# Performance work log

Hardware: AMD Instinct MI355X
Metric: run time of the kernel (lower is better)

## Reference

```python
import jax, jax.numpy as jnp
import numpy as np

SX, SY, C, K = 256, 256, 3, 15
DD, DT, SIGMA = 5, 0.2, 0.65
C0 = tuple(i % C for i in range(K))
C1 = tuple(tuple(i for i in range(K) if i % C == c) for c in range(C))
MA = DD - SIGMA  # flow magnitude bound


def _sobel(A):
    # A: (X, Y, c) -> (X, Y, 2, c); matches jsp.signal.convolve2d(..., mode='same')
    kx = jnp.array([[1., 0., -1.], [2., 0., -2.], [1., 0., -1.]], dtype=A.dtype)
    ky = kx.T
    # convolve2d flips the kernel; emulate true convolution by correlating with rot180 kernels
    kern = jnp.stack([jnp.rot90(ky, 2), jnp.rot90(kx, 2)])[:, None]  # (2,1,3,3): [grad_y, grad_x]
    x = jnp.transpose(A, (2, 0, 1))[:, None]                          # (c,1,X,Y)
    out = jax.lax.conv_general_dilated(x, kern, (1, 1), 'SAME')       # (c,2,X,Y)
    return jnp.transpose(out, (2, 3, 1, 0))                           # (X,Y,2,c)


def _reintegration(A, P, F):
    # Reintegration tracking, has_hidden=True, border='wall', mix='softmax'
    xs, ys = jnp.meshgrid(jnp.arange(SX), jnp.arange(SY))
    pos = (jnp.dstack((ys, xs)) + .5).astype(A.dtype)     # (X,Y,2) cell centers (row, col)
    mus = pos[..., None] + jnp.clip(DT * F, -MA, MA)      # (X,Y,2,C) target centers
    mus = jnp.clip(mus, SIGMA, SX - SIGMA)                # wall border
    shifts = jnp.array([(dx, dy) for dx in range(-DD, DD + 1) for dy in range(-DD, DD + 1)])
    cap = min(1., 2 * SIGMA)

    def step(sft):
        sh = (sft[0], sft[1])
        Ar = jnp.roll(A, sh, axis=(0, 1))
        Pr = jnp.roll(P, sh, axis=(0, 1))
        mur = jnp.roll(mus, sh, axis=(0, 1))
        dpmu = jnp.abs(pos[..., None] - mur)              # (X,Y,2,C)
        sz = .5 - dpmu + SIGMA
        area = jnp.prod(jnp.clip(sz, 0., cap), axis=2) / (4 * SIGMA ** 2)  # (X,Y,C)
        return Ar * area, Pr

    nA, nP = jax.vmap(step)(shifts)                       # (N,X,Y,C), (N,X,Y,K)
    expnA = jnp.exp(nA.sum(-1, keepdims=True)) - 1.       # softmax mix rule
    newA = nA.sum(0)
    newP = (nP * expnA).sum(0) / (expnA.sum(0) + 1e-10)
    return newA, newP


def _forward(A, P, fK_real, fK_imag, m, s):
    fK = fK_real + 1j * fK_imag                           # (X,Y,K) kernel FFTs
    fA = jnp.fft.fft2(A, axes=(0, 1))                     # (X,Y,C)
    fAk = jnp.take(fA, jnp.array(C0), axis=2)             # (X,Y,K) per-kernel source channel
    U = jnp.real(jnp.fft.ifft2(fK * fAk, axes=(0, 1)))    # (X,Y,K)
    U = (2. * jnp.exp(-((U - m) ** 2) / (2. * s ** 2)) - 1.) * P  # growth(U,m,s)*P
    U = jnp.dstack([U[:, :, C1[c]].sum(-1) for c in range(C)])    # (X,Y,C)
    F = _sobel(U)                                         # (X,Y,2,C)
    Cg = _sobel(A.sum(-1, keepdims=True))                 # (X,Y,2,1)
    alpha = jnp.clip((A[:, :, None, :] / 2.) ** 2, 0., 1.)
    F = jnp.clip(F * (1. - alpha) - Cg * alpha, -MA, MA)
    return _reintegration(A, P, F)


def setup_inputs() -> dict:
    key = jax.random.key(0)
    kA, kP, kr, km, ks, ka, kb, kw = jax.random.split(key, 8)
    A = jax.random.uniform(kA, (SX, SY, C), dtype=jnp.float32)
    P = jax.random.uniform(kP, (SX, SY, K), dtype=jnp.float32)
    R = 15.0
    r = jax.random.uniform(kr, (K,), minval=.2, maxval=1.)
    m = jax.random.uniform(km, (K,), minval=.05, maxval=.5, dtype=jnp.float32)
    s = jax.random.uniform(ks, (K,), minval=.001, maxval=.18, dtype=jnp.float32)
    a = jax.random.uniform(ka, (K, 3))
    b = jax.random.uniform(kb, (K, 3), minval=.001, maxval=1.)
    w = jax.random.uniform(kw, (K, 3), minval=.01, maxval=.5)
    mid = SX // 2
    D = jnp.linalg.norm(jnp.mgrid[-mid:mid, -mid:mid], axis=0)[..., None] / ((R + 15.) * r)  # (X,Y,K)
    Kk = jax.nn.sigmoid(-(D - 1.) * 10.) * (b * jnp.exp(-((D[..., None] - a) / w) ** 2)).sum(-1)
    nK = Kk / Kk.sum((0, 1), keepdims=True)
    fK = jnp.fft.fft2(jnp.fft.fftshift(nK, axes=(0, 1)), axes=(0, 1))
    return {"A": A, "P": P,
            "fK_real": jnp.real(fK).astype(jnp.float32),
            "fK_imag": jnp.imag(fK).astype(jnp.float32),
            "m": m, "s": s}


def reference(A, P, fK_real, fK_imag, m, s):
    return _forward(A, P, fK_real, fK_imag, m, s)
```

## Files before the change

### kernel.cpp

```cpp
#include <hip/hip_runtime.h>


#define XY  65536
#define NC  3
#define NK  15
#define WPAD 260

__device__ __forceinline__ float2 cmul(float2 a, float2 b) {
  return make_float2(a.x * b.x - a.y * b.y, a.x * b.y + a.y * b.x);
}

__device__ __forceinline__ void fft256_lds(float2* b0, float2* b1, int t, float sign) {
  float2* src = b0;
  float2* dst = b1;
#pragma unroll
  for (int stage = 0; stage < 4; ++stage) {
    __syncthreads();
    const int Ns = 1 << (2 * stage);
    float2 v0 = src[t];
    float2 v1 = src[t + 64];
    float2 v2 = src[t + 128];
    float2 v3 = src[t + 192];
    const int jm = t & (Ns - 1);
    float ang = sign * 6.283185307179586f * (float)jm / (float)(Ns * 4);
    float sn, cs;
    __sincosf(ang, &sn, &cs);
    float2 w1 = make_float2(cs, sn);
    float2 w2 = cmul(w1, w1);
    float2 w3 = cmul(w2, w1);
    v1 = cmul(v1, w1);
    v2 = cmul(v2, w2);
    v3 = cmul(v3, w3);
    float2 a0 = make_float2(v0.x + v2.x, v0.y + v2.y);
    float2 a1 = make_float2(v0.x - v2.x, v0.y - v2.y);
    float2 a2 = make_float2(v1.x + v3.x, v1.y + v3.y);
    float2 a3 = make_float2(v1.x - v3.x, v1.y - v3.y);
    float2 ia3 = make_float2(-sign * a3.y, sign * a3.x);
    const int idxD = ((t >> (2 * stage)) << (2 * stage)) * 4 + jm;
    dst[idxD]          = make_float2(a0.x + a2.x, a0.y + a2.y);
    dst[idxD + Ns]     = make_float2(a1.x + ia3.x, a1.y + ia3.y);
    dst[idxD + 2 * Ns] = make_float2(a0.x - a2.x, a0.y - a2.y);
    dst[idxD + 3 * Ns] = make_float2(a1.x - ia3.x, a1.y - ia3.y);
    float2* tmp = src; src = dst; dst = tmp;
  }
  __syncthreads();
}

__global__ __launch_bounds__(64) void k_rowfft(const float* __restrict__ A,
                                               float2* __restrict__ RF) {
  __shared__ float2 b0[256], b1[256];
  const int t = threadIdx.x;
  const int x = blockIdx.x & 255;
  const int c = blockIdx.x >> 8;
#pragma unroll
  for (int r = 0; r < 4; ++r) {
    int y = t + 64 * r;
    b0[y] = make_float2(A[(x * 256 + y) * NC + c], 0.0f);
  }
  fft256_lds(b0, b1, t, -1.0f);
#pragma unroll
  for (int r = 0; r < 4; ++r) {
    int y = t + 64 * r;
    RF[(c * 256 + x) * 256 + y] = b0[y];
  }
}

__global__ __launch_bounds__(512, 1) void k_colfft(const float* __restrict__ fKr,
                                                   const float* __restrict__ fKi,
                                                   const float2* __restrict__ RF,
                                                   float2* __restrict__ T2) {
  __shared__ float2 lds0[8 * WPAD];
  __shared__ float2 lds1[8 * WPAD];
  const int tid = threadIdx.x;
  const int k = blockIdx.x >> 5;
  const int y0 = (blockIdx.x & 31) << 3;
  const int c = k % 3;

  {
    const int q = tid & 3;
#pragma unroll
    for (int r = 0; r < 2; ++r) {
      const int x = (tid >> 2) + (r << 7);
      const float4* src = (const float4*)(RF + (c * XY + x * 256 + y0));
      float4 v = src[q];
      lds0[(2 * q) * WPAD + x]     = make_float2(v.x, v.y);
      lds0[(2 * q + 1) * WPAD + x] = make_float2(v.z, v.w);
    }
  }

  const int w = tid >> 6, lane = tid & 63;
  float2* b0 = lds0 + w * WPAD;
  float2* b1 = lds1 + w * WPAD;
  fft256_lds(b0, b1, lane, -1.0f);

  const int y = y0 + w;
  float2 fa[4];
#pragma unroll
  for (int r = 0; r < 4; ++r) fa[r] = b0[lane + 64 * r];
#pragma unroll
  for (int r = 0; r < 4; ++r) {
    const int x = lane + 64 * r;
    const int fi = (x * 256 + y) * NK + k;
    float2 Kv = make_float2(fKr[fi], fKi[fi]);
    b0[x] = cmul(Kv, fa[r]);
  }
  fft256_lds(b0, b1, lane, 1.0f);

  {
    const int q = tid & 3;
#pragma unroll
    for (int r = 0; r < 2; ++r) {
      const int x = (tid >> 2) + (r << 7);
      float2 v0 = lds0[(2 * q) * WPAD + x];
      float2 v1 = lds0[(2 * q + 1) * WPAD + x];
      float4* dst = (float4*)(T2 + (k * XY + x * 256 + y0));
      dst[q] = make_float4(v0.x, v0.y, v1.x, v1.y);
    }
  }
}

__global__ __launch_bounds__(320, 1) void k_irowfft_growth(const float2* __restrict__ T2,
                                                           const float* __restrict__ P,
                                                           const float* __restrict__ m,
                                                           const float* __restrict__ s,
                                                           float* __restrict__ Ucol) {
  __shared__ float2 lds0[5 * WPAD];
  __shared__ float2 lds1[5 * WPAD];
  __shared__ float accs[5 * WPAD];
  const int tid = threadIdx.x;
  const int x = blockIdx.x & 255;
  const int c = blockIdx.x >> 8;
  const int j = tid >> 6, lane = tid & 63;
  const int k = c + 3 * j;

  float2* b0 = lds0 + j * WPAD;
  float2* b1 = lds1 + j * WPAD;
  const float2* src = T2 + (k * XY + x * 256);
#pragma unroll
  for (int r = 0; r < 4; ++r) {
    int y = lane + 64 * r;
    b0[y] = src[y];
  }
  fft256_lds(b0, b1, lane, 1.0f);

  const float mk = m[k];
  const float sk = s[k];
  const float inv2s2 = 0.5f / (sk * sk);
#pragma unroll
  for (int r = 0; r < 4; ++r) {
    int y = lane + 64 * r;
    float U = b0[y].x * (1.0f / 65536.0f);
    float d = U - mk;
    float g = 2.0f * __expf(-d * d * inv2s2) - 1.0f;
    accs[j * WPAD + y] = g * P[(x * 256 + y) * NK + k];
  }
  __syncthreads();
  if (tid < 256) {
    float sum = 0.f;
#pragma unroll
    for (int j2 = 0; j2 < 5; ++j2) sum += accs[j2 * WPAD + tid];
    Ucol[c * XY + x * 256 + tid] = sum;
  }
}

__global__ __launch_bounds__(256) void k_flow(const float* __restrict__ A,
                                              const float* __restrict__ Ucol,
                                              float* __restrict__ F) {
  const int idx = blockIdx.x * 256 + threadIdx.x;
  const int x = idx >> 8;
  const int y = idx & 255;
  const float MA = 4.35f;

  float u[3][3][3];
  float asum[3][3];
#pragma unroll
  for (int di = -1; di <= 1; ++di) {
#pragma unroll
    for (int dj = -1; dj <= 1; ++dj) {
      int xi = x + di, yj = y + dj;
      bool inb = ((unsigned)xi < 256u) && ((unsigned)yj < 256u);
      float a0 = 0.f, a1 = 0.f, a2 = 0.f, as = 0.f;
      if (inb) {
        int b = xi * 256 + yj;
        a0 = Ucol[0 * XY + b];
        a1 = Ucol[1 * XY + b];
        a2 = Ucol[2 * XY + b];
        const float* ap = A + b * NC;
        as = ap[0] + ap[1] + ap[2];
      }
      u[0][di + 1][dj + 1] = a0;
      u[1][di + 1][dj + 1] = a1;
      u[2][di + 1][dj + 1] = a2;
      asum[di + 1][dj + 1] = as;
    }
  }
  float cg0 = (asum[2][0] + 2.f * asum[2][1] + asum[2][2]) -
              (asum[0][0] + 2.f * asum[0][1] + asum[0][2]);
  float cg1 = (asum[0][2] + 2.f * asum[1][2] + asum[2][2]) -
              (asum[0][0] + 2.f * asum[1][0] + asum[2][0]);
  const int b = x * 256 + y;
#pragma unroll
  for (int c = 0; c < NC; ++c) {
    float f0 = (u[c][2][0] + 2.f * u[c][2][1] + u[c][2][2]) -
               (u[c][0][0] + 2.f * u[c][0][1] + u[c][0][2]);
    float f1 = (u[c][0][2] + 2.f * u[c][1][2] + u[c][2][2]) -
               (u[c][0][0] + 2.f * u[c][1][0] + u[c][2][0]);
    float ah = A[b * NC + c] * 0.5f;
    float al = fminf(ah * ah, 1.0f);
    f0 = fminf(fmaxf(f0 * (1.f - al) - cg0 * al, -MA), MA);
    f1 = fminf(fmaxf(f1 * (1.f - al) - cg1 * al, -MA), MA);
    F[(b * 2 + 0) * NC + c] = f0;
    F[(b * 2 + 1) * NC + c] = f1;
  }
}

__global__ __launch_bounds__(256) void k_reint(const float* __restrict__ A,
                                               const float* __restrict__ P,
                                               const float* __restrict__ F,
                                               float* __restrict__ outA,
                                               float* __restrict__ outP) {
  const int idx = blockIdx.x * 256 + threadIdx.x;
  const int x = idx >> 8;
  const int y = idx & 255;
  const float SIGMA = 0.65f;
  const float INV4S2 = 1.0f / (4.0f * 0.65f * 0.65f);
  const float DT = 0.2f;
  const float px = x + 0.5f;
  const float py = y + 0.5f;

  float accA[3] = {0.f, 0.f, 0.f};
  float accP[15];
#pragma unroll
  for (int k = 0; k < NK; ++k) accP[k] = 0.f;
  float esum = 0.f;

  for (int dx = -2; dx <= 2; ++dx) {
    for (int dy = -2; dy <= 2; ++dy) {
      const int sx = (x - dx) & 255;
      const int sy = (y - dy) & 255;
      const int sb = sx * 256 + sy;
      const float spx = sx + 0.5f;
      const float spy = sy + 0.5f;
      float sumnA = 0.f;
      float nAc[3];
#pragma unroll
      for (int c = 0; c < NC; ++c) {
        float f0 = F[(sb * 2 + 0) * NC + c];
        float f1 = F[(sb * 2 + 1) * NC + c];
        float mu0 = fminf(fmaxf(spx + DT * f0, SIGMA), 256.f - SIGMA);
        float mu1 = fminf(fmaxf(spy + DT * f1, SIGMA), 256.f - SIGMA);
        float sz0 = 0.5f - fabsf(px - mu0) + SIGMA;
        float sz1 = 0.5f - fabsf(py - mu1) + SIGMA;
        sz0 = fminf(fmaxf(sz0, 0.f), 1.f);
        sz1 = fminf(fmaxf(sz1, 0.f), 1.f);
        float area = sz0 * sz1 * INV4S2;
        float na = A[sb * NC + c] * area;
        nAc[c] = na;
        sumnA += na;
      }
      float e = __expf(sumnA) - 1.0f;
      accA[0] += nAc[0];
      accA[1] += nAc[1];
      accA[2] += nAc[2];
      esum += e;
      const float* pp = P + sb * NK;
#pragma unroll
      for (int k = 0; k < NK; ++k) accP[k] += pp[k] * e;
    }
  }
  const int b = x * 256 + y;
#pragma unroll
  for (int c = 0; c < NC; ++c) outA[b * NC + c] = accA[c];
  const float inv = 1.0f / (esum + 1e-10f);
#pragma unroll
  for (int k = 0; k < NK; ++k) outP[b * NK + k] = accP[k] * inv;
}

extern "C" void kernel_launch(void* const* d_in, const int* in_sizes, int n_in,
                              void* d_out, int out_size, void* d_ws, size_t ws_size,
                              hipStream_t stream) {
  const float* A   = (const float*)d_in[0];
  const float* P   = (const float*)d_in[1];
  const float* fKr = (const float*)d_in[2];
  const float* fKi = (const float*)d_in[3];
  const float* m   = (const float*)d_in[4];
  const float* s   = (const float*)d_in[5];

  float* ws = (float*)d_ws;
  float2* RF   = (float2*)ws;
  float2* T2   = RF + NC * XY;
  float*  Ucol = (float*)(T2 + NK * XY);
  float*  F    = Ucol + NC * XY;

  float* outA = (float*)d_out;
  float* outP = outA + NC * XY;

  k_rowfft<<<NC * 256, 64, 0, stream>>>(A, RF);
  k_colfft<<<NK * 32, 512, 0, stream>>>(fKr, fKi, RF, T2);
  k_irowfft_growth<<<NC * 256, 320, 0, stream>>>(T2, P, m, s, Ucol);
  k_flow<<<256, 256, 0, stream>>>(A, Ucol, F);
  k_reint<<<256, 256, 0, stream>>>(A, P, F, outA, outP);
}
```

Before: 107.3 us.

## Transpose A, P and F to planar layout and batch row FFTs

Adds a prep kernel that converts interleaved A and P into planar per-channel arrays and precomputes the channel sum of A. Row FFT, growth, flow and reintegration kernels then read coalesced planar data, and F is stored planar. The row FFT now runs four rows per 256-thread block instead of one row per 64-thread block. The cost is an extra kernel launch and an extra pass over P and A, in exchange for coalesced gathers in the reintegration loop, which reads P 25 times per cell.

New measurement: 111.3 us. 1.04x slower.

```diff
diff --git a/kernel.cpp b/kernel.cpp
--- a/kernel.cpp
+++ b/kernel.cpp
@@ -46,21 +46,40 @@
   __syncthreads();
 }
 
-__global__ __launch_bounds__(64) void k_rowfft(const float* __restrict__ A,
-                                               float2* __restrict__ RF) {
-  __shared__ float2 b0[256], b1[256];
-  const int t = threadIdx.x;
-  const int x = blockIdx.x & 255;
-  const int c = blockIdx.x >> 8;
-#pragma unroll
-  for (int r = 0; r < 4; ++r) {
-    int y = t + 64 * r;
-    b0[y] = make_float2(A[(x * 256 + y) * NC + c], 0.0f);
-  }
-  fft256_lds(b0, b1, t, -1.0f);
-#pragma unroll
-  for (int r = 0; r < 4; ++r) {
-    int y = t + 64 * r;
+__global__ __launch_bounds__(256) void k_prep(const float* __restrict__ A,
+                                              const float* __restrict__ P,
+                                              float* __restrict__ Aplan,
+                                              float* __restrict__ Asum,
+                                              float* __restrict__ Pplan) {
+  const int b = blockIdx.x * 256 + threadIdx.x;
+  float a0 = A[b * 3 + 0], a1 = A[b * 3 + 1], a2 = A[b * 3 + 2];
+  Aplan[0 * XY + b] = a0;
+  Aplan[1 * XY + b] = a1;
+  Aplan[2 * XY + b] = a2;
+  Asum[b] = a0 + a1 + a2;
+#pragma unroll
+  for (int k = 0; k < NK; ++k) Pplan[k * XY + b] = P[b * NK + k];
+}
+
+__global__ __launch_bounds__(256) void k_rowfft(const float* __restrict__ Aplan,
+                                                float2* __restrict__ RF) {
+  __shared__ float2 lds0[4 * WPAD], lds1[4 * WPAD];
+  const int tid = threadIdx.x;
+  const int w = tid >> 6, lane = tid & 63;
+  const int c = blockIdx.x >> 6;
+  const int x = ((blockIdx.x & 63) << 2) + w;
+  float2* b0 = lds0 + w * WPAD;
+  float2* b1 = lds1 + w * WPAD;
+  const float* src = Aplan + c * XY + x * 256;
+#pragma unroll
+  for (int r = 0; r < 4; ++r) {
+    int y = lane + 64 * r;
+    b0[y] = make_float2(src[y], 0.0f);
+  }
+  fft256_lds(b0, b1, lane, -1.0f);
+#pragma unroll
+  for (int r = 0; r < 4; ++r) {
+    int y = lane + 64 * r;
     RF[(c * 256 + x) * 256 + y] = b0[y];
   }
 }
@@ -120,7 +139,7 @@
 }
 
 __global__ __launch_bounds__(320, 1) void k_irowfft_growth(const float2* __restrict__ T2,
-                                                           const float* __restrict__ P,
+                                                           const float* __restrict__ Pplan,
                                                            const float* __restrict__ m,
                                                            const float* __restrict__ s,
                                                            float* __restrict__ Ucol) {
@@ -146,13 +165,14 @@
   const float mk = m[k];
   const float sk = s[k];
   const float inv2s2 = 0.5f / (sk * sk);
+  const float* pk = Pplan + k * XY + x * 256;
 #pragma unroll
   for (int r = 0; r < 4; ++r) {
     int y = lane + 64 * r;
     float U = b0[y].x * (1.0f / 65536.0f);
     float d = U - mk;
     float g = 2.0f * __expf(-d * d * inv2s2) - 1.0f;
-    accs[j * WPAD + y] = g * P[(x * 256 + y) * NK + k];
+    accs[j * WPAD + y] = g * pk[y];
   }
   __syncthreads();
   if (tid < 256) {
@@ -163,41 +183,41 @@
   }
 }
 
-__global__ __launch_bounds__(256) void k_flow(const float* __restrict__ A,
+__global__ __launch_bounds__(256) void k_flow(const float* __restrict__ Aplan,
+                                              const float* __restrict__ Asum,
                                               const float* __restrict__ Ucol,
-                                              float* __restrict__ F) {
+                                              float* __restrict__ Fplan) {
   const int idx = blockIdx.x * 256 + threadIdx.x;
   const int x = idx >> 8;
   const int y = idx & 255;
   const float MA = 4.35f;
 
   float u[3][3][3];
-  float asum[3][3];
+  float as[3][3];
 #pragma unroll
   for (int di = -1; di <= 1; ++di) {
 #pragma unroll
     for (int dj = -1; dj <= 1; ++dj) {
       int xi = x + di, yj = y + dj;
       bool inb = ((unsigned)xi < 256u) && ((unsigned)yj < 256u);
-      float a0 = 0.f, a1 = 0.f, a2 = 0.f, as = 0.f;
+      float a0 = 0.f, a1 = 0.f, a2 = 0.f, asv = 0.f;
       if (inb) {
         int b = xi * 256 + yj;
         a0 = Ucol[0 * XY + b];
         a1 = Ucol[1 * XY + b];
         a2 = Ucol[2 * XY + b];
-        const float* ap = A + b * NC;
-        as = ap[0] + ap[1] + ap[2];
+        asv = Asum[b];
       }
       u[0][di + 1][dj + 1] = a0;
       u[1][di + 1][dj + 1] = a1;
       u[2][di + 1][dj + 1] = a2;
-      asum[di + 1][dj + 1] = as;
+      as[di + 1][dj + 1] = asv;
     }
   }
-  float cg0 = (asum[2][0] + 2.f * asum[2][1] + asum[2][2]) -
-              (asum[0][0] + 2.f * asum[0][1] + asum[0][2]);
-  float cg1 = (asum[0][2] + 2.f * asum[1][2] + asum[2][2]) -
-              (asum[0][0] + 2.f * asum[1][0] + asum[2][0]);
+  float cg0 = (as[2][0] + 2.f * as[2][1] + as[2][2]) -
+              (as[0][0] + 2.f * as[0][1] + as[0][2]);
+  float cg1 = (as[0][2] + 2.f * as[1][2] + as[2][2]) -
+              (as[0][0] + 2.f * as[1][0] + as[2][0]);
   const int b = x * 256 + y;
 #pragma unroll
   for (int c = 0; c < NC; ++c) {
@@ -205,18 +225,18 @@
                (u[c][0][0] + 2.f * u[c][0][1] + u[c][0][2]);
     float f1 = (u[c][0][2] + 2.f * u[c][1][2] + u[c][2][2]) -
                (u[c][0][0] + 2.f * u[c][1][0] + u[c][2][0]);
-    float ah = A[b * NC + c] * 0.5f;
+    float ah = Aplan[c * XY + b] * 0.5f;
     float al = fminf(ah * ah, 1.0f);
     f0 = fminf(fmaxf(f0 * (1.f - al) - cg0 * al, -MA), MA);
     f1 = fminf(fmaxf(f1 * (1.f - al) - cg1 * al, -MA), MA);
-    F[(b * 2 + 0) * NC + c] = f0;
-    F[(b * 2 + 1) * NC + c] = f1;
-  }
-}
-
-__global__ __launch_bounds__(256) void k_reint(const float* __restrict__ A,
-                                               const float* __restrict__ P,
-                                               const float* __restrict__ F,
+    Fplan[(0 * 3 + c) * XY + b] = f0;
+    Fplan[(1 * 3 + c) * XY + b] = f1;
+  }
+}
+
+__global__ __launch_bounds__(256) void k_reint(const float* __restrict__ Aplan,
+                                               const float* __restrict__ Pplan,
+                                               const float* __restrict__ Fplan,
                                                float* __restrict__ outA,
                                                float* __restrict__ outP) {
   const int idx = blockIdx.x * 256 + threadIdx.x;
@@ -245,8 +265,8 @@
       float nAc[3];
 #pragma unroll
       for (int c = 0; c < NC; ++c) {
-        float f0 = F[(sb * 2 + 0) * NC + c];
-        float f1 = F[(sb * 2 + 1) * NC + c];
+        float f0 = Fplan[(0 * 3 + c) * XY + sb];
+        float f1 = Fplan[(1 * 3 + c) * XY + sb];
         float mu0 = fminf(fmaxf(spx + DT * f0, SIGMA), 256.f - SIGMA);
         float mu1 = fminf(fmaxf(spy + DT * f1, SIGMA), 256.f - SIGMA);
         float sz0 = 0.5f - fabsf(px - mu0) + SIGMA;
@@ -254,7 +274,7 @@
         sz0 = fminf(fmaxf(sz0, 0.f), 1.f);
         sz1 = fminf(fmaxf(sz1, 0.f), 1.f);
         float area = sz0 * sz1 * INV4S2;
-        float na = A[sb * NC + c] * area;
+        float na = Aplan[c * XY + sb] * area;
         nAc[c] = na;
         sumnA += na;
       }
@@ -263,9 +283,8 @@
       accA[1] += nAc[1];
       accA[2] += nAc[2];
       esum += e;
-      const float* pp = P + sb * NK;
-#pragma unroll
-      for (int k = 0; k < NK; ++k) accP[k] += pp[k] * e;
+#pragma unroll
+      for (int k = 0; k < NK; ++k) accP[k] += Pplan[k * XY + sb] * e;
     }
   }
   const int b = x * 256 + y;
@@ -287,17 +306,21 @@
   const float* s   = (const float*)d_in[5];
 
   float* ws = (float*)d_ws;
-  float2* RF   = (float2*)ws;
-  float2* T2   = RF + NC * XY;
-  float*  Ucol = (float*)(T2 + NK * XY);
-  float*  F    = Ucol + NC * XY;
+  float2* RF    = (float2*)ws;
+  float2* T2    = RF + NC * XY;
+  float*  Ucol  = (float*)(T2 + NK * XY);
+  float*  Fplan = Ucol + NC * XY;
+  float*  Aplan = Fplan + 6 * XY;
+  float*  Asum  = Aplan + NC * XY;
+  float*  Pplan = Asum + XY;
 
   float* outA = (float*)d_out;
   float* outP = outA + NC * XY;
 
-  k_rowfft<<<NC * 256, 64, 0, stream>>>(A, RF);
+  k_prep<<<256, 256, 0, stream>>>(A, P, Aplan, Asum, Pplan);
+  k_rowfft<<<NC * 64, 256, 0, stream>>>(Aplan, RF);
   k_colfft<<<NK * 32, 512, 0, stream>>>(fKr, fKi, RF, T2);
-  k_irowfft_growth<<<NC * 256, 320, 0, stream>>>(T2, P, m, s, Ucol);
-  k_flow<<<256, 256, 0, stream>>>(A, Ucol, F);
-  k_reint<<<256, 256, 0, stream>>>(A, P, F, outA, outP);
-}
+  k_irowfft_growth<<<NC * 256, 320, 0, stream>>>(T2, Pplan, m, s, Ucol);
+  k_flow<<<256, 256, 0, stream>>>(Aplan, Asum, Ucol, Fplan);
+  k_reint<<<256, 256, 0, stream>>>(Aplan, Pplan, Fplan, outA, outP);
+}
```
